# Performance work log

Measured on AMD Instinct MI355X. Metric: run time of the kernel, lower is better.

Reference implementation:

```python
import jax, jax.numpy as jnp
import numpy as np

HID = 128
EDGE_FEAT = 4
NUM_G = 20
CUTOFF = 10.0
N_NODES = 20000
N_EDGES = 640000


def setup_inputs() -> dict:
    key = jax.random.key(0)
    ks = jax.random.split(key, 20)
    s = 0.02
    in_e = 2 * HID + EDGE_FEAT + NUM_G  # 280
    inp = {
        "h": jax.random.normal(ks[0], (N_NODES, HID), jnp.float32),
        "x": jax.random.normal(ks[1], (N_NODES, 3), jnp.float32),
        "edge_attr": jax.random.normal(ks[2], (N_EDGES, EDGE_FEAT), jnp.float32),
        "edge_index": jax.random.randint(ks[3], (2, N_EDGES), 0, N_NODES, jnp.int32),
        "mask_ligand": jax.random.randint(ks[4], (N_NODES,), 0, 2, jnp.int32),
        # edge_mlp: 2 linear layers, silu after both (act_last=True)
        "W_e1": jax.random.normal(ks[5], (in_e, HID), jnp.float32) * s,
        "b_e1": jnp.zeros((HID,), jnp.float32),
        "W_e2": jax.random.normal(ks[6], (HID, HID), jnp.float32) * s,
        "b_e2": jnp.zeros((HID,), jnp.float32),
        # edge gate: Linear(hidden,1) + sigmoid
        "W_g": jax.random.normal(ks[7], (HID, 1), jnp.float32) * s,
        "b_g": jnp.zeros((1,), jnp.float32),
        # node_mlp: Linear -> silu -> Linear (no act last)
        "W_n1": jax.random.normal(ks[8], (2 * HID, HID), jnp.float32) * s,
        "b_n1": jnp.zeros((HID,), jnp.float32),
        "W_n2": jax.random.normal(ks[9], (HID, HID), jnp.float32) * s,
        "b_n2": jnp.zeros((HID,), jnp.float32),
        # x_mlp: Linear -> silu -> Linear(no bias, tiny init) -> tanh
        "W_x1": jax.random.normal(ks[10], (HID, HID), jnp.float32) * s,
        "b_x1": jnp.zeros((HID,), jnp.float32),
        "W_x2": jax.random.normal(ks[11], (HID, 1), jnp.float32) * 0.001,
    }
    return inp


def reference(h, x, edge_attr, W_e1, b_e1, W_e2, b_e2, W_g, b_g,
              W_n1, b_n1, W_n2, b_n2, W_x1, b_x1, W_x2,
              edge_index, mask_ligand):
    src, dst = edge_index[0], edge_index[1]
    rel = x[dst] - x[src]                                # [E,3]
    d2 = jnp.sum(rel * rel, axis=-1, keepdims=True)     # [E,1]
    r = jnp.sqrt(d2 + 1e-8)
    # Gaussian smearing RBF
    offset = jnp.linspace(0.0, CUTOFF, NUM_G)
    coeff = -0.5 / (offset[1] - offset[0]) ** 2
    d_feat = jnp.exp(coeff * (r - offset) ** 2)          # [E,NUM_G]
    m_in = jnp.concatenate([h[dst], h[src], d_feat, edge_attr], axis=-1)
    m = jax.nn.silu(m_in @ W_e1 + b_e1)
    m = jax.nn.silu(m @ W_e2 + b_e2)
    g = jax.nn.sigmoid(m @ W_g + b_g)                    # [E,1]
    msg = m * g
    agg = jnp.zeros((h.shape[0], HID), msg.dtype).at[dst].add(msg)
    nm = jax.nn.silu(jnp.concatenate([agg, h], axis=-1) @ W_n1 + b_n1)
    h_out = h + (nm @ W_n2 + b_n2)
    coef = jnp.tanh(jax.nn.silu(m @ W_x1 + b_x1) @ W_x2)  # [E,1]
    vec = rel / (r + 1.0) * coef
    dx = jnp.zeros_like(x).at[dst].add(vec.astype(x.dtype))
    x_out = x + dx * mask_ligand.astype(x.dtype)[:, None]
    return (h_out, x_out)
```

## Files before the change

### kernel.cpp

```cpp
#include <hip/hip_runtime.h>
#include <hip/hip_bf16.h>
#include <math.h>

#define HID 128
#define NUM_G 20
#define EF 4
#define NN 20000
#define NE 640000
#define KN1 256

typedef __attribute__((ext_vector_type(8))) short short8;
typedef __attribute__((ext_vector_type(4))) short short4v;
typedef __attribute__((ext_vector_type(4))) float floatx4;
typedef __attribute__((ext_vector_type(4))) unsigned int uintx4;

__device__ __forceinline__ float silu_f(float v){
    return v * __builtin_amdgcn_rcpf(1.0f + __expf(-v));
}
__device__ __forceinline__ float sigm_f(float v){
    return __builtin_amdgcn_rcpf(1.0f + __expf(-v));
}
__device__ __forceinline__ float tanh_f(float v){
    return 1.0f - 2.0f * __builtin_amdgcn_rcpf(1.0f + __expf(2.0f * v));
}
__device__ __forceinline__ unsigned short f2bf(float v){
    unsigned int u = __float_as_uint(v);
    u = (u + 0x7fffu + ((u >> 16) & 1u)) >> 16;
    return (unsigned short)u;
}
__device__ __forceinline__ float bf2f(unsigned short u){
    return __uint_as_float(((unsigned int)u) << 16);
}
__device__ __forceinline__ unsigned int pk2(float a, float b){
    __hip_bfloat162 h = __float22bfloat162_rn(make_float2(a, b));
    return *(unsigned int*)&h;
}
__device__ __forceinline__ unsigned long long pk4(float a, float b, float c, float d){
    return (unsigned long long)pk2(a, b) | ((unsigned long long)pk2(c, d) << 32);
}
__device__ __forceinline__ float2 up2(unsigned int u){
    __hip_bfloat162 h = *(__hip_bfloat162*)&u;
    return __bfloat1622float2(h);
}

__global__ __launch_bounds__(320) void prep_hist_kernel(
    const float* __restrict__ W_e1, const float* __restrict__ W_e2,
    const float* __restrict__ W_x1, const float* __restrict__ W_n1,
    const float* __restrict__ W_n2,
    unsigned short* __restrict__ WT1d, unsigned short* __restrict__ WT1s,
    unsigned short* __restrict__ WT1r,
    unsigned short* __restrict__ WT_e2, unsigned short* __restrict__ WT_x1,
    unsigned short* __restrict__ WT_n1, unsigned short* __restrict__ WT_n2,
    const int* __restrict__ edge_index, int* __restrict__ counts)
{
    int t = threadIdx.x;
    if (blockIdx.x < 128) {
        int n = blockIdx.x;
        if (t < HID) {
            WT1d[n*HID + t] = f2bf(W_e1[t*HID + n]);
            WT1s[n*HID + t] = f2bf(W_e1[(HID+t)*HID + n]);
            WT_e2[n*HID + t] = f2bf(W_e2[t*HID + n]);
            WT_x1[n*HID + t] = f2bf(W_x1[t*HID + n]);
            WT_n2[n*HID + t] = f2bf(W_n2[t*HID + n]);
        }
        if (t < 32) WT1r[n*32 + t] = (t < NUM_G+EF) ? f2bf(W_e1[(256+t)*HID + n]) : (unsigned short)0;
        if (t < KN1) WT_n1[n*KN1 + t] = f2bf(W_n1[t*HID + n]);
    } else {
        int e = (blockIdx.x - 128) * 320 + t;
        atomicAdd(&counts[edge_index[NE + e]], 1);
    }
}

__global__ __launch_bounds__(1024) void scan_kernel(
    const int* __restrict__ counts, int* __restrict__ cursor)
{
    __shared__ int part[1024];
    const int t = threadIdx.x;
    const int CH = (NN + 1023) / 1024;
    int base = t * CH;
    int s = 0;
    for (int i = 0; i < CH; ++i) { int idx = base + i; if (idx < NN) s += counts[idx]; }
    part[t] = s; __syncthreads();
    for (int off = 1; off < 1024; off <<= 1) {
        int v = (t >= off) ? part[t - off] : 0;
        __syncthreads();
        part[t] += v;
        __syncthreads();
    }
    int run = (t == 0) ? 0 : part[t - 1];
    for (int i = 0; i < CH; ++i) {
        int idx = base + i;
        if (idx < NN) { cursor[idx] = run; run += counts[idx]; }
    }
}

#define PD_BLOCKS ((NN + 63) / 64)
__global__ __launch_bounds__(256) void build_pd_kernel(
    const int* __restrict__ edge_index, const float* __restrict__ x,
    const float* __restrict__ edge_attr, int* __restrict__ cursor,
    uintx4* __restrict__ rec,
    const float* __restrict__ h, const float* __restrict__ b_e1,
    const unsigned short* __restrict__ WT1d, const unsigned short* __restrict__ WT1s,
    unsigned short* __restrict__ PD, unsigned short* __restrict__ PS)
{
    if (blockIdx.x >= PD_BLOCKS) {
        int e = (blockIdx.x - PD_BLOCKS) * 256 + threadIdx.x;
        int s = edge_index[e];
        int d = edge_index[NE + e];
        int pos = atomicAdd(&cursor[d], 1);
        float rx = x[d*3+0] - x[s*3+0];
        float ry = x[d*3+1] - x[s*3+1];
        float rz = x[d*3+2] - x[s*3+2];
        float r  = sqrtf(rx*rx + ry*ry + rz*rz + 1e-8f);
        uintx4 lo, hi;
        lo[0] = (unsigned int)s; lo[1] = (unsigned int)d;
        lo[2] = __float_as_uint(rx); lo[3] = __float_as_uint(ry);
        hi[0] = __float_as_uint(rz); hi[1] = __float_as_uint(r);
        hi[2] = (unsigned int)f2bf(edge_attr[(size_t)e*EF + 0])
              | ((unsigned int)f2bf(edge_attr[(size_t)e*EF + 1]) << 16);
        hi[3] = (unsigned int)f2bf(edge_attr[(size_t)e*EF + 2])
              | ((unsigned int)f2bf(edge_attr[(size_t)e*EF + 3]) << 16);
        rec[(size_t)pos*2]     = lo;
        rec[(size_t)pos*2 + 1] = hi;
        return;
    }

    const int wv   = threadIdx.x >> 6;
    const int lane = threadIdx.x & 63;
    const int quad = lane >> 4;
    const int l15  = lane & 15;
    int node = blockIdx.x * 64 + wv * 16 + l15;
    if (node >= NN) node = NN - 1;

    short8 ah[4];
    #pragma unroll
    for (int kc = 0; kc < 4; ++kc) {
        const float* p = h + (size_t)node*HID + kc*32 + quad*8;
        float4 f0 = *(const float4*)(p);
        float4 f1 = *(const float4*)(p + 4);
        uintx4 u;
        u[0] = pk2(f0.x, f0.y); u[1] = pk2(f0.z, f0.w);
        u[2] = pk2(f1.x, f1.y); u[3] = pk2(f1.z, f1.w);
        ah[kc] = __builtin_bit_cast(short8, u);
    }

    floatx4 ad[8], as8[8];
    #pragma unroll
    for (int t = 0; t < 8; ++t) {
        float4 bb = *(const float4*)(b_e1 + t*16 + quad*4);
        ad[t]  = (floatx4){bb.x, bb.y, bb.z, bb.w};
        as8[t] = (floatx4){0.f, 0.f, 0.f, 0.f};
    }
    #pragma unroll
    for (int kc = 0; kc < 4; ++kc) {
        #pragma unroll
        for (int t = 0; t < 8; ++t) {
            short8 bd = *(const short8*)(WT1d + (size_t)(t*16+l15)*HID + kc*32 + quad*8);
            short8 bs = *(const short8*)(WT1s + (size_t)(t*16+l15)*HID + kc*32 + quad*8);
            ad[t]  = __builtin_amdgcn_mfma_f32_16x16x32_bf16(bd, ah[kc], ad[t], 0, 0, 0);
            as8[t] = __builtin_amdgcn_mfma_f32_16x16x32_bf16(bs, ah[kc], as8[t], 0, 0, 0);
        }
    }
    #pragma unroll
    for (int t = 0; t < 8; ++t) {
        *(unsigned long long*)(PD + (size_t)node*HID + t*16 + quad*4) =
            pk4(ad[t][0], ad[t][1], ad[t][2], ad[t][3]);
        *(unsigned long long*)(PS + (size_t)node*HID + t*16 + quad*4) =
            pk4(as8[t][0], as8[t][1], as8[t][2], as8[t][3]);
    }
}

__global__ __launch_bounds__(128, 3) void egnn_edge_mfma(
    const uintx4* __restrict__ rec,
    const unsigned short* __restrict__ PD, const unsigned short* __restrict__ PS,
    const unsigned short* __restrict__ WT1r,
    const unsigned short* __restrict__ WT_e2,
    const unsigned short* __restrict__ WT_x1,
    const float* __restrict__ b_e2,
    const float* __restrict__ W_g,  const float* __restrict__ b_g,
    const float* __restrict__ b_x1, const float* __restrict__ W_x2,
    float* __restrict__ agg, float* __restrict__ dxv)
{
    __shared__ __align__(16) unsigned short T[2][32*HID];
    __shared__ float s_g[2][32];
    __shared__ float s_vec[2][96];

    const int wv   = threadIdx.x >> 6;
    const int lane = threadIdx.x & 63;
    const int quad = lane >> 4;
    const int l15  = lane & 15;
    const int bid  = (int)(blockIdx.x & 7) * 1250 + (int)(blockIdx.x >> 3);
    const int e0   = (bid * 2 + wv) * 32;

    char* Tb = (char*)&T[wv][0];
    const int rsw = (l15 & 7) << 4;

    int   sreg = 0, dreg = 0;
    float rxr = 0.f, ryr = 0.f, rzr = 0.f, rreg = 0.f;
    unsigned int au01 = 0, au23 = 0;
    if (lane < 32) {
        uintx4 lo = rec[(size_t)(e0 + lane)*2];
        uintx4 hi = rec[(size_t)(e0 + lane)*2 + 1];
        sreg = (int)lo[0]; dreg = (int)lo[1];
        rxr = __uint_as_float(lo[2]); ryr = __uint_as_float(lo[3]);
        rzr = __uint_as_float(hi[0]); rreg = __uint_as_float(hi[1]);
        au01 = hi[2]; au23 = hi[3];
    }
    int nxt = __shfl(dreg, lane + 1);
    const unsigned int bmask =
        (unsigned int)__ballot(lane < 32 && (lane == 31 || dreg != nxt));

    const int   nd0 = __shfl(dreg, l15);
    const int   ns0 = __shfl(sreg, l15);
    const float rr0 = __shfl(rreg, l15);
    const int   nd1 = __shfl(dreg, 16 + l15);
    const int   ns1 = __shfl(sreg, 16 + l15);
    const float rr1 = __shfl(rreg, 16 + l15);
    const unsigned int at01_0 = __shfl(au01, l15),      at23_0 = __shfl(au23, l15);
    const unsigned int at01_1 = __shfl(au01, 16 + l15), at23_1 = __shfl(au23, 16 + l15);

    short8 pdv0[4], psv0[4], pdv1[4], psv1[4];
    #pragma unroll
    for (int kc = 0; kc < 4; ++kc) {
        pdv0[kc] = *(const short8*)(PD + (size_t)nd0*HID + kc*32 + quad*8);
        psv0[kc] = *(const short8*)(PS + (size_t)ns0*HID + kc*32 + quad*8);
        pdv1[kc] = *(const short8*)(PD + (size_t)nd1*HID + kc*32 + quad*8);
        psv1[kc] = *(const short8*)(PS + (size_t)ns1*HID + kc*32 + quad*8);
    }

    short8 ar0, ar1;
    {
        const float step  = 10.0f / 19.0f;
        const float coeff = -0.5f / (step*step);
        uintx4 u0, u1;
        #pragma unroll
        for (int jp = 0; jp < 4; ++jp) {
            float v[4];
            #pragma unroll
            for (int half = 0; half < 2; ++half) {
                float rr = half ? rr1 : rr0;
                #pragma unroll
                for (int q = 0; q < 2; ++q) {
                    int col = quad*8 + jp*2 + q;
                    float val = 0.f;
                    if (col < NUM_G) {
                        float d = rr - step*(float)col;
                        val = __expf(coeff*d*d);
                    } else if (col < NUM_G+EF) {
                        unsigned int w = (col < 22) ? (half ? at01_1 : at01_0)
                                                    : (half ? at23_1 : at23_0);
                        val = bf2f((unsigned short)((col & 1) ? (w >> 16) : (w & 0xffffu)));
                    }
                    v[half*2 + q] = val;
                }
            }
            u0[jp] = pk2(v[0], v[1]);
            u1[jp] = pk2(v[2], v[3]);
        }
        ar0 = __builtin_bit_cast(short8, u0);
        ar1 = __builtin_bit_cast(short8, u1);
    }

    floatx4 acc0[8], acc1[8];
    #pragma unroll
    for (int t = 0; t < 8; ++t) { acc0[t] = (floatx4){0,0,0,0}; acc1[t] = (floatx4){0,0,0,0}; }
    #pragma unroll
    for (int t = 0; t < 8; ++t) {
        short8 b = *(const short8*)(WT1r + (size_t)(t*16+l15)*32 + quad*8);
        acc0[t] = __builtin_amdgcn_mfma_f32_16x16x32_bf16(b, ar0, acc0[t], 0, 0, 0);
        acc1[t] = __builtin_amdgcn_mfma_f32_16x16x32_bf16(b, ar1, acc1[t], 0, 0, 0);
    }
    #pragma unroll
    for (int t = 0; t < 8; ++t) {
        int bc = (t*16 + quad*4) * 2;
        *(unsigned long long*)(Tb + l15*256      + (bc ^ rsw)) =
            pk4(acc0[t][0], acc0[t][1], acc0[t][2], acc0[t][3]);
        *(unsigned long long*)(Tb + (16+l15)*256 + (bc ^ rsw)) =
            pk4(acc1[t][0], acc1[t][1], acc1[t][2], acc1[t][3]);
    }
    __builtin_amdgcn_wave_barrier();

    #pragma unroll
    for (int t = 0; t < 8; ++t) {
        float4 bb = *(const float4*)(b_e2 + t*16 + quad*4);
        acc0[t] = (floatx4){bb.x, bb.y, bb.z, bb.w};
        acc1[t] = acc0[t];
    }
    __builtin_amdgcn_s_setprio(1);
    #pragma unroll
    for (int kc = 0; kc < 4; ++kc) {
        int bc = (kc*32 + quad*8) * 2;
        uintx4 rv0 = __builtin_bit_cast(uintx4, *(const short8*)(Tb + l15*256      + (bc ^ rsw)));
        uintx4 rv1 = __builtin_bit_cast(uintx4, *(const short8*)(Tb + (16+l15)*256 + (bc ^ rsw)));
        uintx4 pu0 = __builtin_bit_cast(uintx4, pdv0[kc]);
        uintx4 su0 = __builtin_bit_cast(uintx4, psv0[kc]);
        uintx4 pu1 = __builtin_bit_cast(uintx4, pdv1[kc]);
        uintx4 su1 = __builtin_bit_cast(uintx4, psv1[kc]);
        uintx4 o0, o1;
        #pragma unroll
        for (int w = 0; w < 4; ++w) {
            float2 p0 = up2(pu0[w]), s0 = up2(su0[w]), r0 = up2(rv0[w]);
            float2 p1 = up2(pu1[w]), s1 = up2(su1[w]), r1 = up2(rv1[w]);
            o0[w] = pk2(silu_f(p0.x + s0.x + r0.x), silu_f(p0.y + s0.y + r0.y));
            o1[w] = pk2(silu_f(p1.x + s1.x + r1.x), silu_f(p1.y + s1.y + r1.y));
        }
        short8 a2t0 = __builtin_bit_cast(short8, o0);
        short8 a2t1 = __builtin_bit_cast(short8, o1);
        #pragma unroll
        for (int t = 0; t < 8; ++t) {
            short8 b = *(const short8*)(WT_e2 + (size_t)(t*16+l15)*HID + kc*32 + quad*8);
            acc0[t] = __builtin_amdgcn_mfma_f32_16x16x32_bf16(b, a2t0, acc0[t], 0, 0, 0);
            acc1[t] = __builtin_amdgcn_mfma_f32_16x16x32_bf16(b, a2t1, acc1[t], 0, 0, 0);
        }
    }
    __builtin_amdgcn_s_setprio(0);

    {
        float gp0 = 0.f, gp1 = 0.f;
        #pragma unroll
        for (int t = 0; t < 8; ++t) {
            float4 wg = *(const float4*)(W_g + t*16 + quad*4);
            float m0 = silu_f(acc0[t][0]), m1 = silu_f(acc0[t][1]);
            float m2v = silu_f(acc0[t][2]), m3 = silu_f(acc0[t][3]);
            float n0v = silu_f(acc1[t][0]), n1 = silu_f(acc1[t][1]);
            float n2 = silu_f(acc1[t][2]),  n3 = silu_f(acc1[t][3]);
            gp0 += m0*wg.x + m1*wg.y + m2v*wg.z + m3*wg.w;
            gp1 += n0v*wg.x + n1*wg.y + n2*wg.z + n3*wg.w;
            int bc = (t*16 + quad*4) * 2;
            *(unsigned long long*)(Tb + l15*256      + (bc ^ rsw)) = pk4(m0, m1, m2v, m3);
            *(unsigned long long*)(Tb + (16+l15)*256 + (bc ^ rsw)) = pk4(n0v, n1, n2, n3);
        }
        gp0 += __shfl_xor(gp0, 16); gp0 += __shfl_xor(gp0, 32);
        gp1 += __shfl_xor(gp1, 16); gp1 += __shfl_xor(gp1, 32);
        if (lane < 16) {
            const float bg0 = b_g[0];
            s_g[wv][l15]      = sigm_f(gp0 + bg0);
            s_g[wv][16 + l15] = sigm_f(gp1 + bg0);
        }
    }
    __builtin_amdgcn_wave_barrier();

    #pragma unroll
    for (int t = 0; t < 8; ++t) {
        float4 bb = *(const float4*)(b_x1 + t*16 + quad*4);
        acc0[t] = (floatx4){bb.x, bb.y, bb.z, bb.w};
        acc1[t] = acc0[t];
    }
    {
        float am0 = 0.f, am1 = 0.f;
        __builtin_amdgcn_s_setprio(1);
        #pragma unroll
        for (int kc = 0; kc < 4; ++kc) {
            #pragma unroll
            for (int r8 = 0; r8 < 8; ++r8) {
                int r = kc*8 + r8;
                unsigned int pv = *(const unsigned int*)(Tb + r*256 + ((lane*4) ^ ((r&7)<<4)));
                float gr = s_g[wv][r];
                float2 f = up2(pv);
                am0 += f.x * gr;
                am1 += f.y * gr;
                if (bmask & (1u << r)) {
                    int dr = __shfl(dreg, r);
                    atomicAdd(&agg[(size_t)dr*HID + lane*2],     am0);
                    atomicAdd(&agg[(size_t)dr*HID + lane*2 + 1], am1);
                    am0 = 0.f; am1 = 0.f;
                }
            }
            int bc = (kc*32 + quad*8) * 2;
            short8 a3t0 = *(const short8*)(Tb + l15*256      + (bc ^ rsw));
            short8 a3t1 = *(const short8*)(Tb + (16+l15)*256 + (bc ^ rsw));
            #pragma unroll
            for (int t = 0; t < 8; ++t) {
                short8 b = *(const short8*)(WT_x1 + (size_t)(t*16+l15)*HID + kc*32 + quad*8);
                acc0[t] = __builtin_amdgcn_mfma_f32_16x16x32_bf16(b, a3t0, acc0[t], 0, 0, 0);
                acc1[t] = __builtin_amdgcn_mfma_f32_16x16x32_bf16(b, a3t1, acc1[t], 0, 0, 0);
            }
        }
        __builtin_amdgcn_s_setprio(0);
    }

    {
        float cp0 = 0.f, cp1 = 0.f;
        #pragma unroll
        for (int t = 0; t < 8; ++t) {
            float4 wx = *(const float4*)(W_x2 + t*16 + quad*4);
            cp0 += silu_f(acc0[t][0])*wx.x + silu_f(acc0[t][1])*wx.y
                 + silu_f(acc0[t][2])*wx.z + silu_f(acc0[t][3])*wx.w;
            cp1 += silu_f(acc1[t][0])*wx.x + silu_f(acc1[t][1])*wx.y
                 + silu_f(acc1[t][2])*wx.z + silu_f(acc1[t][3])*wx.w;
        }
        cp0 += __shfl_xor(cp0, 16); cp0 += __shfl_xor(cp0, 32);
        cp1 += __shfl_xor(cp1, 16); cp1 += __shfl_xor(cp1, 32);
        if (quad < 2) {
            int el = quad*16 + l15;
            float cp = (quad == 0) ? cp0 : cp1;
            float co = tanh_f(cp);
            float rx = __shfl(rxr, el), ry = __shfl(ryr, el), rz = __shfl(rzr, el);
            float rv = __shfl(rreg, el);
            float sc = __builtin_amdgcn_rcpf(rv + 1.0f) * co;
            s_vec[wv][el*3 + 0] = rx * sc;
            s_vec[wv][el*3 + 1] = ry * sc;
            s_vec[wv][el*3 + 2] = rz * sc;
        }
    }
    __builtin_amdgcn_wave_barrier();

    {
        float a = 0.f;
        #pragma unroll
        for (int r = 0; r < 32; ++r) {
            float vv = (lane < 3) ? s_vec[wv][r*3 + lane] : 0.f;
            a += vv;
            if (bmask & (1u << r)) {
                int dr = __shfl(dreg, r);
                if (lane < 3) atomicAdd(&dxv[(size_t)dr*3 + lane], a);
                a = 0.f;
            }
        }
    }
}

__global__ __launch_bounds__(64, 4) void egnn_node_mfma(
    const float* __restrict__ h, const float* __restrict__ x,
    const int* __restrict__ mask,
    const float* __restrict__ agg, const float* __restrict__ dxv,
    const unsigned short* __restrict__ WT_n1, const float* __restrict__ b_n1,
    const unsigned short* __restrict__ WT_n2, const float* __restrict__ b_n2,
    float* __restrict__ h_out, float* __restrict__ x_out)
{
    __shared__ __align__(16) unsigned short T[16*HID];

    const int lane = threadIdx.x;
    const int quad = lane >> 4;
    const int l15  = lane & 15;
    const int n0   = blockIdx.x * 16;
    char* Tb = (char*)T;
    const int rsw = (l15 & 7) << 4;

    if (lane < 48) {
        int r = lane / 3, c = lane % 3;
        int n = n0 + r;
        x_out[n*3 + c] = x[n*3 + c] + dxv[n*3 + c] * (float)mask[n];
    }

    const int node = n0 + l15;
    short8 a1[8];
    #pragma unroll
    for (int kc = 0; kc < 4; ++kc) {
        const float* p = agg + (size_t)node*HID + kc*32 + quad*8;
        float4 f0 = *(const float4*)(p);
        float4 f1 = *(const float4*)(p + 4);
        uintx4 u;
        u[0] = pk2(f0.x, f0.y); u[1] = pk2(f0.z, f0.w);
        u[2] = pk2(f1.x, f1.y); u[3] = pk2(f1.z, f1.w);
        a1[kc] = __builtin_bit_cast(short8, u);
    }
    #pragma unroll
    for (int kc = 0; kc < 4; ++kc) {
        const float* p = h + (size_t)node*HID + kc*32 + quad*8;
        float4 f0 = *(const float4*)(p);
        float4 f1 = *(const float4*)(p + 4);
        uintx4 u;
        u[0] = pk2(f0.x, f0.y); u[1] = pk2(f0.z, f0.w);
        u[2] = pk2(f1.x, f1.y); u[3] = pk2(f1.z, f1.w);
        a1[4+kc] = __builtin_bit_cast(short8, u);
    }

    floatx4 acc[8];
    #pragma unroll
    for (int t = 0; t < 8; ++t) {
        float4 bb = *(const float4*)(b_n1 + t*16 + quad*4);
        acc[t] = (floatx4){bb.x, bb.y, bb.z, bb.w};
    }
    #pragma unroll
    for (int kc = 0; kc < 8; ++kc) {
        #pragma unroll
        for (int t = 0; t < 8; ++t) {
            short8 b = *(const short8*)(WT_n1 + (size_t)(t*16+l15)*KN1 + kc*32 + quad*8);
            acc[t] = __builtin_amdgcn_mfma_f32_16x16x32_bf16(b, a1[kc], acc[t], 0, 0, 0);
        }
    }
    #pragma unroll
    for (int t = 0; t < 8; ++t) {
        int bc = (t*16 + quad*4) * 2;
        *(unsigned long long*)(Tb + l15*256 + (bc ^ rsw)) =
            pk4(silu_f(acc[t][0]), silu_f(acc[t][1]), silu_f(acc[t][2]), silu_f(acc[t][3]));
    }
    __builtin_amdgcn_wave_barrier();

    short8 a2[4];
    #pragma unroll
    for (int kc = 0; kc < 4; ++kc) {
        int bc = (kc*32 + quad*8) * 2;
        a2[kc] = *(const short8*)(Tb + l15*256 + (bc ^ rsw));
    }
    #pragma unroll
    for (int t = 0; t < 8; ++t) {
        float4 hv = *(const float4*)(h + (size_t)node*HID + t*16 + quad*4);
        float4 bb = *(const float4*)(b_n2 + t*16 + quad*4);
        acc[t] = (floatx4){hv.x + bb.x, hv.y + bb.y, hv.z + bb.z, hv.w + bb.w};
    }
    #pragma unroll
    for (int kc = 0; kc < 4; ++kc) {
        #pragma unroll
        for (int t = 0; t < 8; ++t) {
            short8 b = *(const short8*)(WT_n2 + (size_t)(t*16+l15)*HID + kc*32 + quad*8);
            acc[t] = __builtin_amdgcn_mfma_f32_16x16x32_bf16(b, a2[kc], acc[t], 0, 0, 0);
        }
    }
    #pragma unroll
    for (int t = 0; t < 8; ++t) {
        *(floatx4*)(h_out + (size_t)node*HID + t*16 + quad*4) = acc[t];
    }
}

extern "C" void kernel_launch(void* const* d_in, const int* in_sizes, int n_in,
                              void* d_out, int out_size, void* d_ws, size_t ws_size,
                              hipStream_t stream) {
    const float* h          = (const float*)d_in[0];
    const float* x          = (const float*)d_in[1];
    const float* edge_attr  = (const float*)d_in[2];
    const int*   edge_index = (const int*)  d_in[3];
    const int*   mask       = (const int*)  d_in[4];
    const float* W_e1 = (const float*)d_in[5];
    const float* b_e1 = (const float*)d_in[6];
    const float* W_e2 = (const float*)d_in[7];
    const float* b_e2 = (const float*)d_in[8];
    const float* W_g  = (const float*)d_in[9];
    const float* b_g  = (const float*)d_in[10];
    const float* W_n1 = (const float*)d_in[11];
    const float* b_n1 = (const float*)d_in[12];
    const float* W_n2 = (const float*)d_in[13];
    const float* b_n2 = (const float*)d_in[14];
    const float* W_x1 = (const float*)d_in[15];
    const float* b_x1 = (const float*)d_in[16];
    const float* W_x2 = (const float*)d_in[17];

    char* ws = (char*)d_ws;
    float* agg = (float*)ws;                       ws += (size_t)NN*HID*4;
    float* dxv = (float*)ws;                       ws += (size_t)NN*3*4;
    int*   counts = (int*)ws;                      ws += (size_t)NN*4;
    int*   cursor = (int*)ws;                      ws += (size_t)NN*4;
    uintx4* rec   = (uintx4*)ws;                   ws += (size_t)NE*32;
    unsigned short* PD    = (unsigned short*)ws;   ws += (size_t)NN*HID*2;
    unsigned short* PS    = (unsigned short*)ws;   ws += (size_t)NN*HID*2;
    unsigned short* WT1d  = (unsigned short*)ws;   ws += (size_t)HID*HID*2;
    unsigned short* WT1s  = (unsigned short*)ws;   ws += (size_t)HID*HID*2;
    unsigned short* WT1r  = (unsigned short*)ws;   ws += (size_t)HID*32*2;
    unsigned short* WT_e2 = (unsigned short*)ws;   ws += (size_t)HID*HID*2;
    unsigned short* WT_x1 = (unsigned short*)ws;   ws += (size_t)HID*HID*2;
    unsigned short* WT_n1 = (unsigned short*)ws;   ws += (size_t)HID*KN1*2;
    unsigned short* WT_n2 = (unsigned short*)ws;   ws += (size_t)HID*HID*2;

    hipMemsetAsync(agg, 0, ((size_t)NN*HID + (size_t)NN*3)*sizeof(float), stream);
    hipMemsetAsync(counts, 0, (size_t)NN*sizeof(int), stream);

    prep_hist_kernel<<<128 + NE/320, 320, 0, stream>>>(
        W_e1, W_e2, W_x1, W_n1, W_n2,
        WT1d, WT1s, WT1r, WT_e2, WT_x1, WT_n1, WT_n2,
        edge_index, counts);

    scan_kernel<<<1, 1024, 0, stream>>>(counts, cursor);

    build_pd_kernel<<<PD_BLOCKS + NE/256, 256, 0, stream>>>(
        edge_index, x, edge_attr, cursor, rec,
        h, b_e1, WT1d, WT1s, PD, PS);

    egnn_edge_mfma<<<NE/64, 128, 0, stream>>>(
        rec, PD, PS, WT1r, WT_e2, WT_x1,
        b_e2, W_g, b_g, b_x1, W_x2, agg, dxv);

    float* h_out = (float*)d_out;
    float* x_out = h_out + (size_t)NN*HID;

    egnn_node_mfma<<<NN/16, 64, 0, stream>>>(
        h, x, mask, agg, dxv, WT_n1, b_n1, WT_n2, b_n2, h_out, x_out);
}
```

Measured before the change: 502.9 us.

## Process edge tiles sequentially to cut registers; fold agg zeroing into prep kernel

The edge kernel no longer carries two 16-edge tiles through every stage together. It now loops over the two tiles one after the other, so only one set of accumulators and one set of gathered PD/PS rows is live at a time. The second tile's PD/PS gathers are issued during the first tile's compute, which lowers register pressure and may raise occupancy, at the cost of less MFMA interleaving between independent tiles. Separately, the hipMemset of agg/dxv is replaced by extra blocks in the prep/histogram kernel that write zeros, removing one memset launch. The gated aggregation runs only after the second tile, once all 32 rows are in LDS.

Result: slower. 701.8 us (+39.6%).

```diff
diff --git a/kernel.cpp b/kernel.cpp
--- a/kernel.cpp
+++ b/kernel.cpp
@@ -51,7 +51,8 @@
     unsigned short* __restrict__ WT1r,
     unsigned short* __restrict__ WT_e2, unsigned short* __restrict__ WT_x1,
     unsigned short* __restrict__ WT_n1, unsigned short* __restrict__ WT_n2,
-    const int* __restrict__ edge_index, int* __restrict__ counts)
+    const int* __restrict__ edge_index, int* __restrict__ counts,
+    float4* __restrict__ zero_base)
 {
     int t = threadIdx.x;
     if (blockIdx.x < 128) {
@@ -65,9 +66,12 @@
         }
         if (t < 32) WT1r[n*32 + t] = (t < NUM_G+EF) ? f2bf(W_e1[(256+t)*HID + n]) : (unsigned short)0;
         if (t < KN1) WT_n1[n*KN1 + t] = f2bf(W_n1[t*HID + n]);
-    } else {
+    } else if (blockIdx.x < 2128) {
         int e = (blockIdx.x - 128) * 320 + t;
         atomicAdd(&counts[edge_index[NE + e]], 1);
+    } else {
+        int idx = (blockIdx.x - 2128) * 320 + t;
+        if (idx < (NN*HID + NN*3)/4) zero_base[idx] = make_float4(0.f,0.f,0.f,0.f);
     }
 }
 
@@ -210,35 +214,32 @@
     const unsigned int bmask =
         (unsigned int)__ballot(lane < 32 && (lane == 31 || dreg != nxt));
 
-    const int   nd0 = __shfl(dreg, l15);
-    const int   ns0 = __shfl(sreg, l15);
-    const float rr0 = __shfl(rreg, l15);
-    const int   nd1 = __shfl(dreg, 16 + l15);
-    const int   ns1 = __shfl(sreg, 16 + l15);
-    const float rr1 = __shfl(rreg, 16 + l15);
-    const unsigned int at01_0 = __shfl(au01, l15),      at23_0 = __shfl(au23, l15);
-    const unsigned int at01_1 = __shfl(au01, 16 + l15), at23_1 = __shfl(au23, 16 + l15);
-
-    short8 pdv0[4], psv0[4], pdv1[4], psv1[4];
-    #pragma unroll
-    for (int kc = 0; kc < 4; ++kc) {
-        pdv0[kc] = *(const short8*)(PD + (size_t)nd0*HID + kc*32 + quad*8);
-        psv0[kc] = *(const short8*)(PS + (size_t)ns0*HID + kc*32 + quad*8);
-        pdv1[kc] = *(const short8*)(PD + (size_t)nd1*HID + kc*32 + quad*8);
-        psv1[kc] = *(const short8*)(PS + (size_t)ns1*HID + kc*32 + quad*8);
-    }
-
-    short8 ar0, ar1;
+    short8 pdv[4], psv[4];
     {
-        const float step  = 10.0f / 19.0f;
-        const float coeff = -0.5f / (step*step);
-        uintx4 u0, u1;
-        #pragma unroll
-        for (int jp = 0; jp < 4; ++jp) {
-            float v[4];
-            #pragma unroll
-            for (int half = 0; half < 2; ++half) {
-                float rr = half ? rr1 : rr0;
+        const int nd = __shfl(dreg, l15);
+        const int ns = __shfl(sreg, l15);
+        #pragma unroll
+        for (int kc = 0; kc < 4; ++kc) {
+            pdv[kc] = *(const short8*)(PD + (size_t)nd*HID + kc*32 + quad*8);
+            psv[kc] = *(const short8*)(PS + (size_t)ns*HID + kc*32 + quad*8);
+        }
+    }
+
+    #pragma unroll
+    for (int ti = 0; ti < 2; ++ti) {
+        const int rb = ti * 16;
+        const float        rr   = __shfl(rreg, rb + l15);
+        const unsigned int at01 = __shfl(au01, rb + l15);
+        const unsigned int at23 = __shfl(au23, rb + l15);
+
+        short8 ar;
+        {
+            const float step  = 10.0f / 19.0f;
+            const float coeff = -0.5f / (step*step);
+            uintx4 u;
+            #pragma unroll
+            for (int jp = 0; jp < 4; ++jp) {
+                float v[2];
                 #pragma unroll
                 for (int q = 0; q < 2; ++q) {
                     int col = quad*8 + jp*2 + q;
@@ -247,113 +248,112 @@
                         float d = rr - step*(float)col;
                         val = __expf(coeff*d*d);
                     } else if (col < NUM_G+EF) {
-                        unsigned int w = (col < 22) ? (half ? at01_1 : at01_0)
-                                                    : (half ? at23_1 : at23_0);
+                        unsigned int w = (col < 22) ? at01 : at23;
                         val = bf2f((unsigned short)((col & 1) ? (w >> 16) : (w & 0xffffu)));
                     }
-                    v[half*2 + q] = val;
+                    v[q] = val;
                 }
-            }
-            u0[jp] = pk2(v[0], v[1]);
-            u1[jp] = pk2(v[2], v[3]);
-        }
-        ar0 = __builtin_bit_cast(short8, u0);
-        ar1 = __builtin_bit_cast(short8, u1);
-    }
-
-    floatx4 acc0[8], acc1[8];
-    #pragma unroll
-    for (int t = 0; t < 8; ++t) { acc0[t] = (floatx4){0,0,0,0}; acc1[t] = (floatx4){0,0,0,0}; }
-    #pragma unroll
-    for (int t = 0; t < 8; ++t) {
-        short8 b = *(const short8*)(WT1r + (size_t)(t*16+l15)*32 + quad*8);
-        acc0[t] = __builtin_amdgcn_mfma_f32_16x16x32_bf16(b, ar0, acc0[t], 0, 0, 0);
-        acc1[t] = __builtin_amdgcn_mfma_f32_16x16x32_bf16(b, ar1, acc1[t], 0, 0, 0);
-    }
-    #pragma unroll
-    for (int t = 0; t < 8; ++t) {
-        int bc = (t*16 + quad*4) * 2;
-        *(unsigned long long*)(Tb + l15*256      + (bc ^ rsw)) =
-            pk4(acc0[t][0], acc0[t][1], acc0[t][2], acc0[t][3]);
-        *(unsigned long long*)(Tb + (16+l15)*256 + (bc ^ rsw)) =
-            pk4(acc1[t][0], acc1[t][1], acc1[t][2], acc1[t][3]);
-    }
-    __builtin_amdgcn_wave_barrier();
-
-    #pragma unroll
-    for (int t = 0; t < 8; ++t) {
-        float4 bb = *(const float4*)(b_e2 + t*16 + quad*4);
-        acc0[t] = (floatx4){bb.x, bb.y, bb.z, bb.w};
-        acc1[t] = acc0[t];
-    }
-    __builtin_amdgcn_s_setprio(1);
-    #pragma unroll
-    for (int kc = 0; kc < 4; ++kc) {
-        int bc = (kc*32 + quad*8) * 2;
-        uintx4 rv0 = __builtin_bit_cast(uintx4, *(const short8*)(Tb + l15*256      + (bc ^ rsw)));
-        uintx4 rv1 = __builtin_bit_cast(uintx4, *(const short8*)(Tb + (16+l15)*256 + (bc ^ rsw)));
-        uintx4 pu0 = __builtin_bit_cast(uintx4, pdv0[kc]);
-        uintx4 su0 = __builtin_bit_cast(uintx4, psv0[kc]);
-        uintx4 pu1 = __builtin_bit_cast(uintx4, pdv1[kc]);
-        uintx4 su1 = __builtin_bit_cast(uintx4, psv1[kc]);
-        uintx4 o0, o1;
-        #pragma unroll
-        for (int w = 0; w < 4; ++w) {
-            float2 p0 = up2(pu0[w]), s0 = up2(su0[w]), r0 = up2(rv0[w]);
-            float2 p1 = up2(pu1[w]), s1 = up2(su1[w]), r1 = up2(rv1[w]);
-            o0[w] = pk2(silu_f(p0.x + s0.x + r0.x), silu_f(p0.y + s0.y + r0.y));
-            o1[w] = pk2(silu_f(p1.x + s1.x + r1.x), silu_f(p1.y + s1.y + r1.y));
-        }
-        short8 a2t0 = __builtin_bit_cast(short8, o0);
-        short8 a2t1 = __builtin_bit_cast(short8, o1);
-        #pragma unroll
-        for (int t = 0; t < 8; ++t) {
-            short8 b = *(const short8*)(WT_e2 + (size_t)(t*16+l15)*HID + kc*32 + quad*8);
-            acc0[t] = __builtin_amdgcn_mfma_f32_16x16x32_bf16(b, a2t0, acc0[t], 0, 0, 0);
-            acc1[t] = __builtin_amdgcn_mfma_f32_16x16x32_bf16(b, a2t1, acc1[t], 0, 0, 0);
-        }
-    }
-    __builtin_amdgcn_s_setprio(0);
-
-    {
-        float gp0 = 0.f, gp1 = 0.f;
-        #pragma unroll
-        for (int t = 0; t < 8; ++t) {
-            float4 wg = *(const float4*)(W_g + t*16 + quad*4);
-            float m0 = silu_f(acc0[t][0]), m1 = silu_f(acc0[t][1]);
-            float m2v = silu_f(acc0[t][2]), m3 = silu_f(acc0[t][3]);
-            float n0v = silu_f(acc1[t][0]), n1 = silu_f(acc1[t][1]);
-            float n2 = silu_f(acc1[t][2]),  n3 = silu_f(acc1[t][3]);
-            gp0 += m0*wg.x + m1*wg.y + m2v*wg.z + m3*wg.w;
-            gp1 += n0v*wg.x + n1*wg.y + n2*wg.z + n3*wg.w;
+                u[jp] = pk2(v[0], v[1]);
+            }
+            ar = __builtin_bit_cast(short8, u);
+        }
+
+        floatx4 acc[8];
+        #pragma unroll
+        for (int t = 0; t < 8; ++t) acc[t] = (floatx4){0,0,0,0};
+        #pragma unroll
+        for (int t = 0; t < 8; ++t) {
+            short8 b = *(const short8*)(WT1r + (size_t)(t*16+l15)*32 + quad*8);
+            acc[t] = __builtin_amdgcn_mfma_f32_16x16x32_bf16(b, ar, acc[t], 0, 0, 0);
+        }
+        #pragma unroll
+        for (int t = 0; t < 8; ++t) {
             int bc = (t*16 + quad*4) * 2;
-            *(unsigned long long*)(Tb + l15*256      + (bc ^ rsw)) = pk4(m0, m1, m2v, m3);
-            *(unsigned long long*)(Tb + (16+l15)*256 + (bc ^ rsw)) = pk4(n0v, n1, n2, n3);
-        }
-        gp0 += __shfl_xor(gp0, 16); gp0 += __shfl_xor(gp0, 32);
-        gp1 += __shfl_xor(gp1, 16); gp1 += __shfl_xor(gp1, 32);
-        if (lane < 16) {
-            const float bg0 = b_g[0];
-            s_g[wv][l15]      = sigm_f(gp0 + bg0);
-            s_g[wv][16 + l15] = sigm_f(gp1 + bg0);
-        }
-    }
-    __builtin_amdgcn_wave_barrier();
-
-    #pragma unroll
-    for (int t = 0; t < 8; ++t) {
-        float4 bb = *(const float4*)(b_x1 + t*16 + quad*4);
-        acc0[t] = (floatx4){bb.x, bb.y, bb.z, bb.w};
-        acc1[t] = acc0[t];
-    }
-    {
-        float am0 = 0.f, am1 = 0.f;
+            *(unsigned long long*)(Tb + (rb + l15)*256 + (bc ^ rsw)) =
+                pk4(acc[t][0], acc[t][1], acc[t][2], acc[t][3]);
+        }
+        __builtin_amdgcn_wave_barrier();
+
+        short8 a2[4];
+        #pragma unroll
+        for (int kc = 0; kc < 4; ++kc) {
+            int bc = (kc*32 + quad*8) * 2;
+            uintx4 rv = __builtin_bit_cast(uintx4, *(const short8*)(Tb + (rb + l15)*256 + (bc ^ rsw)));
+            uintx4 pu = __builtin_bit_cast(uintx4, pdv[kc]);
+            uintx4 su = __builtin_bit_cast(uintx4, psv[kc]);
+            uintx4 o;
+            #pragma unroll
+            for (int w = 0; w < 4; ++w) {
+                float2 p0 = up2(pu[w]), s0 = up2(su[w]), r0 = up2(rv[w]);
+                o[w] = pk2(silu_f(p0.x + s0.x + r0.x), silu_f(p0.y + s0.y + r0.y));
+            }
+            a2[kc] = __builtin_bit_cast(short8, o);
+        }
+
+        if (ti == 0) {
+            const int nd1 = __shfl(dreg, 16 + l15);
+            const int ns1 = __shfl(sreg, 16 + l15);
+            #pragma unroll
+            for (int kc = 0; kc < 4; ++kc) {
+                pdv[kc] = *(const short8*)(PD + (size_t)nd1*HID + kc*32 + quad*8);
+                psv[kc] = *(const short8*)(PS + (size_t)ns1*HID + kc*32 + quad*8);
+            }
+        }
+
+        #pragma unroll
+        for (int t = 0; t < 8; ++t) {
+            float4 bb = *(const float4*)(b_e2 + t*16 + quad*4);
+            acc[t] = (floatx4){bb.x, bb.y, bb.z, bb.w};
+        }
         __builtin_amdgcn_s_setprio(1);
         #pragma unroll
         for (int kc = 0; kc < 4; ++kc) {
             #pragma unroll
-            for (int r8 = 0; r8 < 8; ++r8) {
-                int r = kc*8 + r8;
+            for (int t = 0; t < 8; ++t) {
+                short8 b = *(const short8*)(WT_e2 + (size_t)(t*16+l15)*HID + kc*32 + quad*8);
+                acc[t] = __builtin_amdgcn_mfma_f32_16x16x32_bf16(b, a2[kc], acc[t], 0, 0, 0);
+            }
+        }
+        __builtin_amdgcn_s_setprio(0);
+
+        {
+            float gp = 0.f;
+            #pragma unroll
+            for (int t = 0; t < 8; ++t) {
+                float4 wg = *(const float4*)(W_g + t*16 + quad*4);
+                float m0 = silu_f(acc[t][0]), m1 = silu_f(acc[t][1]);
+                float m2v = silu_f(acc[t][2]), m3 = silu_f(acc[t][3]);
+                gp += m0*wg.x + m1*wg.y + m2v*wg.z + m3*wg.w;
+                int bc = (t*16 + quad*4) * 2;
+                *(unsigned long long*)(Tb + (rb + l15)*256 + (bc ^ rsw)) = pk4(m0, m1, m2v, m3);
+            }
+            gp += __shfl_xor(gp, 16); gp += __shfl_xor(gp, 32);
+            if (lane < 16) s_g[wv][rb + l15] = sigm_f(gp + b_g[0]);
+        }
+        __builtin_amdgcn_wave_barrier();
+
+        #pragma unroll
+        for (int t = 0; t < 8; ++t) {
+            float4 bb = *(const float4*)(b_x1 + t*16 + quad*4);
+            acc[t] = (floatx4){bb.x, bb.y, bb.z, bb.w};
+        }
+        __builtin_amdgcn_s_setprio(1);
+        #pragma unroll
+        for (int kc = 0; kc < 4; ++kc) {
+            int bc = (kc*32 + quad*8) * 2;
+            short8 a3 = *(const short8*)(Tb + (rb + l15)*256 + (bc ^ rsw));
+            #pragma unroll
+            for (int t = 0; t < 8; ++t) {
+                short8 b = *(const short8*)(WT_x1 + (size_t)(t*16+l15)*HID + kc*32 + quad*8);
+                acc[t] = __builtin_amdgcn_mfma_f32_16x16x32_bf16(b, a3, acc[t], 0, 0, 0);
+            }
+        }
+        __builtin_amdgcn_s_setprio(0);
+
+        if (ti == 1) {
+            float am0 = 0.f, am1 = 0.f;
+            #pragma unroll
+            for (int r = 0; r < 32; ++r) {
                 unsigned int pv = *(const unsigned int*)(Tb + r*256 + ((lane*4) ^ ((r&7)<<4)));
                 float gr = s_g[wv][r];
                 float2 f = up2(pv);
@@ -366,41 +366,27 @@
                     am0 = 0.f; am1 = 0.f;
                 }
             }
-            int bc = (kc*32 + quad*8) * 2;
-            short8 a3t0 = *(const short8*)(Tb + l15*256      + (bc ^ rsw));
-            short8 a3t1 = *(const short8*)(Tb + (16+l15)*256 + (bc ^ rsw));
+        }
+
+        {
+            float cp = 0.f;
             #pragma unroll
             for (int t = 0; t < 8; ++t) {
-                short8 b = *(const short8*)(WT_x1 + (size_t)(t*16+l15)*HID + kc*32 + quad*8);
-                acc0[t] = __builtin_amdgcn_mfma_f32_16x16x32_bf16(b, a3t0, acc0[t], 0, 0, 0);
-                acc1[t] = __builtin_amdgcn_mfma_f32_16x16x32_bf16(b, a3t1, acc1[t], 0, 0, 0);
-            }
-        }
-        __builtin_amdgcn_s_setprio(0);
-    }
-
-    {
-        float cp0 = 0.f, cp1 = 0.f;
-        #pragma unroll
-        for (int t = 0; t < 8; ++t) {
-            float4 wx = *(const float4*)(W_x2 + t*16 + quad*4);
-            cp0 += silu_f(acc0[t][0])*wx.x + silu_f(acc0[t][1])*wx.y
-                 + silu_f(acc0[t][2])*wx.z + silu_f(acc0[t][3])*wx.w;
-            cp1 += silu_f(acc1[t][0])*wx.x + silu_f(acc1[t][1])*wx.y
-                 + silu_f(acc1[t][2])*wx.z + silu_f(acc1[t][3])*wx.w;
-        }
-        cp0 += __shfl_xor(cp0, 16); cp0 += __shfl_xor(cp0, 32);
-        cp1 += __shfl_xor(cp1, 16); cp1 += __shfl_xor(cp1, 32);
-        if (quad < 2) {
-            int el = quad*16 + l15;
-            float cp = (quad == 0) ? cp0 : cp1;
-            float co = tanh_f(cp);
-            float rx = __shfl(rxr, el), ry = __shfl(ryr, el), rz = __shfl(rzr, el);
-            float rv = __shfl(rreg, el);
-            float sc = __builtin_amdgcn_rcpf(rv + 1.0f) * co;
-            s_vec[wv][el*3 + 0] = rx * sc;
-            s_vec[wv][el*3 + 1] = ry * sc;
-            s_vec[wv][el*3 + 2] = rz * sc;
+                float4 wx = *(const float4*)(W_x2 + t*16 + quad*4);
+                cp += silu_f(acc[t][0])*wx.x + silu_f(acc[t][1])*wx.y
+                    + silu_f(acc[t][2])*wx.z + silu_f(acc[t][3])*wx.w;
+            }
+            cp += __shfl_xor(cp, 16); cp += __shfl_xor(cp, 32);
+            if (quad == 0) {
+                int el = rb + l15;
+                float co = tanh_f(cp);
+                float rx = __shfl(rxr, el), ry = __shfl(ryr, el), rz = __shfl(rzr, el);
+                float rv = __shfl(rreg, el);
+                float sc = __builtin_amdgcn_rcpf(rv + 1.0f) * co;
+                s_vec[wv][el*3 + 0] = rx * sc;
+                s_vec[wv][el*3 + 1] = ry * sc;
+                s_vec[wv][el*3 + 2] = rz * sc;
+            }
         }
     }
     __builtin_amdgcn_wave_barrier();
@@ -552,13 +538,12 @@
     unsigned short* WT_n1 = (unsigned short*)ws;   ws += (size_t)HID*KN1*2;
     unsigned short* WT_n2 = (unsigned short*)ws;   ws += (size_t)HID*HID*2;
 
-    hipMemsetAsync(agg, 0, ((size_t)NN*HID + (size_t)NN*3)*sizeof(float), stream);
     hipMemsetAsync(counts, 0, (size_t)NN*sizeof(int), stream);
 
-    prep_hist_kernel<<<128 + NE/320, 320, 0, stream>>>(
+    prep_hist_kernel<<<128 + NE/320 + 2048, 320, 0, stream>>>(
         W_e1, W_e2, W_x1, W_n1, W_n2,
         WT1d, WT1s, WT1r, WT_e2, WT_x1, WT_n1, WT_n2,
-        edge_index, counts);
+        edge_index, counts, (float4*)agg);
 
     scan_kernel<<<1, 1024, 0, stream>>>(counts, cursor);
 
```

## Fold agg memset into prep kernel and restructure edge MFMA phases

Applied to the files above, without the earlier changes.

The large zeroing memset of agg and dxv is removed and done by extra blocks appended to the prep/histogram kernel, which saves one launch. In the edge kernel, the second-layer A operands are now computed into a register array before the MFMA loop, separating the elementwise work from the matrix work. The x_mlp MFMA loop is also split from the gated scatter-add loop, so the atomics no longer interleave with the MFMAs. This raises register pressure (eight short8 values held live) and serialises the atomic phase after the MFMAs.

Measured after the change: 445.1 us. -11.5%, faster.

```diff
diff --git a/kernel.cpp b/kernel.cpp
--- a/kernel.cpp
+++ b/kernel.cpp
@@ -51,7 +51,8 @@
     unsigned short* __restrict__ WT1r,
     unsigned short* __restrict__ WT_e2, unsigned short* __restrict__ WT_x1,
     unsigned short* __restrict__ WT_n1, unsigned short* __restrict__ WT_n2,
-    const int* __restrict__ edge_index, int* __restrict__ counts)
+    const int* __restrict__ edge_index, int* __restrict__ counts,
+    float4* __restrict__ zero_base)
 {
     int t = threadIdx.x;
     if (blockIdx.x < 128) {
@@ -65,9 +66,12 @@
         }
         if (t < 32) WT1r[n*32 + t] = (t < NUM_G+EF) ? f2bf(W_e1[(256+t)*HID + n]) : (unsigned short)0;
         if (t < KN1) WT_n1[n*KN1 + t] = f2bf(W_n1[t*HID + n]);
-    } else {
+    } else if (blockIdx.x < 2128) {
         int e = (blockIdx.x - 128) * 320 + t;
         atomicAdd(&counts[edge_index[NE + e]], 1);
+    } else {
+        int idx = (blockIdx.x - 2128) * 320 + t;
+        if (idx < (NN*HID + NN*3)/4) zero_base[idx] = make_float4(0.f,0.f,0.f,0.f);
     }
 }
 
@@ -280,13 +284,7 @@
     }
     __builtin_amdgcn_wave_barrier();
 
-    #pragma unroll
-    for (int t = 0; t < 8; ++t) {
-        float4 bb = *(const float4*)(b_e2 + t*16 + quad*4);
-        acc0[t] = (floatx4){bb.x, bb.y, bb.z, bb.w};
-        acc1[t] = acc0[t];
-    }
-    __builtin_amdgcn_s_setprio(1);
+    short8 a2[8];
     #pragma unroll
     for (int kc = 0; kc < 4; ++kc) {
         int bc = (kc*32 + quad*8) * 2;
@@ -304,17 +302,28 @@
             o0[w] = pk2(silu_f(p0.x + s0.x + r0.x), silu_f(p0.y + s0.y + r0.y));
             o1[w] = pk2(silu_f(p1.x + s1.x + r1.x), silu_f(p1.y + s1.y + r1.y));
         }
-        short8 a2t0 = __builtin_bit_cast(short8, o0);
-        short8 a2t1 = __builtin_bit_cast(short8, o1);
+        a2[kc]   = __builtin_bit_cast(short8, o0);
+        a2[4+kc] = __builtin_bit_cast(short8, o1);
+    }
+    __builtin_amdgcn_wave_barrier();
+
+    #pragma unroll
+    for (int t = 0; t < 8; ++t) {
+        float4 bb = *(const float4*)(b_e2 + t*16 + quad*4);
+        acc0[t] = (floatx4){bb.x, bb.y, bb.z, bb.w};
+        acc1[t] = acc0[t];
+    }
+    __builtin_amdgcn_s_setprio(1);
+    #pragma unroll
+    for (int kc = 0; kc < 4; ++kc) {
         #pragma unroll
         for (int t = 0; t < 8; ++t) {
             short8 b = *(const short8*)(WT_e2 + (size_t)(t*16+l15)*HID + kc*32 + quad*8);
-            acc0[t] = __builtin_amdgcn_mfma_f32_16x16x32_bf16(b, a2t0, acc0[t], 0, 0, 0);
-            acc1[t] = __builtin_amdgcn_mfma_f32_16x16x32_bf16(b, a2t1, acc1[t], 0, 0, 0);
+            acc0[t] = __builtin_amdgcn_mfma_f32_16x16x32_bf16(b, a2[kc],   acc0[t], 0, 0, 0);
+            acc1[t] = __builtin_amdgcn_mfma_f32_16x16x32_bf16(b, a2[4+kc], acc1[t], 0, 0, 0);
         }
     }
     __builtin_amdgcn_s_setprio(0);
-
     {
         float gp0 = 0.f, gp1 = 0.f;
         #pragma unroll
@@ -341,42 +350,45 @@
     __builtin_amdgcn_wave_barrier();
 
     #pragma unroll
+    for (int kc = 0; kc < 4; ++kc) {
+        int bc = (kc*32 + quad*8) * 2;
+        a2[kc]   = *(const short8*)(Tb + l15*256      + (bc ^ rsw));
+        a2[4+kc] = *(const short8*)(Tb + (16+l15)*256 + (bc ^ rsw));
+    }
+    #pragma unroll
     for (int t = 0; t < 8; ++t) {
         float4 bb = *(const float4*)(b_x1 + t*16 + quad*4);
         acc0[t] = (floatx4){bb.x, bb.y, bb.z, bb.w};
         acc1[t] = acc0[t];
     }
+    __builtin_amdgcn_s_setprio(1);
+    #pragma unroll
+    for (int kc = 0; kc < 4; ++kc) {
+        #pragma unroll
+        for (int t = 0; t < 8; ++t) {
+            short8 b = *(const short8*)(WT_x1 + (size_t)(t*16+l15)*HID + kc*32 + quad*8);
+            acc0[t] = __builtin_amdgcn_mfma_f32_16x16x32_bf16(b, a2[kc],   acc0[t], 0, 0, 0);
+            acc1[t] = __builtin_amdgcn_mfma_f32_16x16x32_bf16(b, a2[4+kc], acc1[t], 0, 0, 0);
+        }
+    }
+    __builtin_amdgcn_s_setprio(0);
+
     {
         float am0 = 0.f, am1 = 0.f;
-        __builtin_amdgcn_s_setprio(1);
-        #pragma unroll
-        for (int kc = 0; kc < 4; ++kc) {
-            #pragma unroll
-            for (int r8 = 0; r8 < 8; ++r8) {
-                int r = kc*8 + r8;
-                unsigned int pv = *(const unsigned int*)(Tb + r*256 + ((lane*4) ^ ((r&7)<<4)));
-                float gr = s_g[wv][r];
-                float2 f = up2(pv);
-                am0 += f.x * gr;
-                am1 += f.y * gr;
-                if (bmask & (1u << r)) {
-                    int dr = __shfl(dreg, r);
-                    atomicAdd(&agg[(size_t)dr*HID + lane*2],     am0);
-                    atomicAdd(&agg[(size_t)dr*HID + lane*2 + 1], am1);
-                    am0 = 0.f; am1 = 0.f;
-                }
+        #pragma unroll
+        for (int r = 0; r < 32; ++r) {
+            unsigned int pv = *(const unsigned int*)(Tb + r*256 + ((lane*4) ^ ((r&7)<<4)));
+            float gr = s_g[wv][r];
+            float2 f = up2(pv);
+            am0 += f.x * gr;
+            am1 += f.y * gr;
+            if (bmask & (1u << r)) {
+                int dr = __shfl(dreg, r);
+                atomicAdd(&agg[(size_t)dr*HID + lane*2],     am0);
+                atomicAdd(&agg[(size_t)dr*HID + lane*2 + 1], am1);
+                am0 = 0.f; am1 = 0.f;
             }
-            int bc = (kc*32 + quad*8) * 2;
-            short8 a3t0 = *(const short8*)(Tb + l15*256      + (bc ^ rsw));
-            short8 a3t1 = *(const short8*)(Tb + (16+l15)*256 + (bc ^ rsw));
-            #pragma unroll
-            for (int t = 0; t < 8; ++t) {
-                short8 b = *(const short8*)(WT_x1 + (size_t)(t*16+l15)*HID + kc*32 + quad*8);
-                acc0[t] = __builtin_amdgcn_mfma_f32_16x16x32_bf16(b, a3t0, acc0[t], 0, 0, 0);
-                acc1[t] = __builtin_amdgcn_mfma_f32_16x16x32_bf16(b, a3t1, acc1[t], 0, 0, 0);
-            }
-        }
-        __builtin_amdgcn_s_setprio(0);
+        }
     }
 
     {
@@ -552,13 +564,12 @@
     unsigned short* WT_n1 = (unsigned short*)ws;   ws += (size_t)HID*KN1*2;
     unsigned short* WT_n2 = (unsigned short*)ws;   ws += (size_t)HID*HID*2;
 
-    hipMemsetAsync(agg, 0, ((size_t)NN*HID + (size_t)NN*3)*sizeof(float), stream);
     hipMemsetAsync(counts, 0, (size_t)NN*sizeof(int), stream);
 
-    prep_hist_kernel<<<128 + NE/320, 320, 0, stream>>>(
+    prep_hist_kernel<<<128 + NE/320 + 2048, 320, 0, stream>>>(
         W_e1, W_e2, W_x1, W_n1, W_n2,
         WT1d, WT1s, WT1r, WT_e2, WT_x1, WT_n1, WT_n2,
-        edge_index, counts);
+        edge_index, counts, (float4*)agg);
 
     scan_kernel<<<1, 1024, 0, stream>>>(counts, cursor);
 
```
